# Kernel tuning notes

Hardware: AMD Instinct MI355X
Metric: run time of the kernel (lower is better)

## Reference

```python
import math
import jax, jax.numpy as jnp
import numpy as np

L, H, K, NH, V, DFF = 6, 512, 512, 8, 64, 1024
B, T, S = 8, 512, 512
PAD = 0


def _ln(x, g, b, eps=1e-5):
    m = jnp.mean(x, -1, keepdims=True)
    v = jnp.mean((x - m) ** 2, -1, keepdims=True)
    return (x - m) * jax.lax.rsqrt(v + eps) * g + b


def _mha(Q, Kin, Vin, mask, wq, bq, wk, bk, wv, bv, wo, bo, g, b):
    # weights stored [in, out]
    B_, Tq, Hd = Q.shape
    dk = wq.shape[1] // NH
    dv = wv.shape[1] // NH
    q = (Q @ wq + bq).reshape(B_, Tq, NH, dk).transpose(0, 2, 1, 3)
    k = (Kin @ wk + bk).reshape(B_, -1, NH, dk).transpose(0, 2, 1, 3)
    v = (Vin @ wv + bv).reshape(B_, -1, NH, dv).transpose(0, 2, 1, 3)
    scores = jnp.einsum('bhqd,bhkd->bhqk', q, k) / jnp.sqrt(jnp.float32(dk))
    scores = jnp.where(mask[:, None, :, :], jnp.float32(-1e9), scores)
    attn = jax.nn.softmax(scores, axis=-1)
    ctx = jnp.einsum('bhqk,bhkd->bhqd', attn, v).transpose(0, 2, 1, 3).reshape(B_, Tq, Hd)
    return _ln(ctx @ wo + bo + Q, g, b)


def _pe(t, d):
    pos = jnp.arange(t, dtype=jnp.float32)[:, None]
    div = jnp.exp(jnp.arange(0, d, 2, dtype=jnp.float32) * (-math.log(10000.0) / d))
    pe = jnp.zeros((t, d), jnp.float32)
    pe = pe.at[:, 0::2].set(jnp.sin(pos * div)).at[:, 1::2].set(jnp.cos(pos * div))
    return pe


def setup_inputs() -> dict:
    key = jax.random.key(0)
    ks = iter(jax.random.split(key, 40))
    nrm = lambda shape, s=0.02: jax.random.normal(next(ks), shape, jnp.float32) * s
    inp = {
        'smiles_index': jax.random.randint(next(ks), (B, T), 0, V, dtype=jnp.int32),
        'enc_outputs': jax.random.normal(next(ks), (B, S, H), jnp.float32),
        'enc_pad_mask': jnp.zeros((B, 1, S), bool),
        'tgt_len': T,
        'mol_emb': nrm((V, H), 1.0).at[PAD].set(0.0),  # padding_idx=0 row zeroed
        # self-attn stacks [L, ...]
        'sa_wq': nrm((L, H, K)), 'sa_bq': jnp.zeros((L, K)),
        'sa_wk': nrm((L, H, K)), 'sa_bk': jnp.zeros((L, K)),
        'sa_wv': nrm((L, H, H)), 'sa_bv': jnp.zeros((L, H)),
        'sa_wo': nrm((L, H, H)), 'sa_bo': jnp.zeros((L, H)),
        'ln1_g': jnp.ones((L, H)), 'ln1_b': jnp.zeros((L, H)),
        # cross-attn stacks
        'ea_wq': nrm((L, H, K)), 'ea_bq': jnp.zeros((L, K)),
        'ea_wk': nrm((L, H, K)), 'ea_bk': jnp.zeros((L, K)),
        'ea_wv': nrm((L, H, H)), 'ea_bv': jnp.zeros((L, H)),
        'ea_wo': nrm((L, H, H)), 'ea_bo': jnp.zeros((L, H)),
        'ln2_g': jnp.ones((L, H)), 'ln2_b': jnp.zeros((L, H)),
        # conv1x1 FFN == per-position linear
        'c1_w': nrm((L, H, DFF)), 'c1_b': jnp.zeros((L, DFF)),
        'c2_w': nrm((L, DFF, H)), 'c2_b': jnp.zeros((L, H)),
        'ln3_g': jnp.ones((L, H)), 'ln3_b': jnp.zeros((L, H)),
    }
    return inp


def reference(smiles_index, enc_outputs, enc_pad_mask, tgt_len, mol_emb,
              sa_wq, sa_bq, sa_wk, sa_bk, sa_wv, sa_bv, sa_wo, sa_bo, ln1_g, ln1_b,
              ea_wq, ea_bq, ea_wk, ea_bk, ea_wv, ea_bv, ea_wo, ea_bo, ln2_g, ln2_b,
              c1_w, c1_b, c2_w, c2_b, ln3_g, ln3_b):
    b, t = smiles_index.shape
    s = enc_outputs.shape[1]
    # embeddings + sinusoidal positional encoding (dropout is identity in eval)
    x = mol_emb[smiles_index] + _pe(t, mol_emb.shape[1])[None]
    # masks: pad (key == pad_id) OR causal upper-triangular
    pad = (smiles_index == PAD)[:, None, :]                 # [B,1,T] -> broadcast over queries
    causal = jnp.triu(jnp.ones((t, t), bool), 1)[None]      # [1,T,T]
    self_mask = pad | causal                                # [B,T,T]
    enc_mask = jnp.broadcast_to(enc_pad_mask, (b, t, s))    # [B,T,S]
    for l in range(L):
        x = _mha(x, x, x, self_mask,
                 sa_wq[l], sa_bq[l], sa_wk[l], sa_bk[l], sa_wv[l], sa_bv[l],
                 sa_wo[l], sa_bo[l], ln1_g[l], ln1_b[l])
        x = _mha(x, enc_outputs, enc_outputs, enc_mask,
                 ea_wq[l], ea_bq[l], ea_wk[l], ea_bk[l], ea_wv[l], ea_bv[l],
                 ea_wo[l], ea_bo[l], ln2_g[l], ln2_b[l])
        h = jax.nn.relu(x @ c1_w[l] + c1_b[l])
        y = h @ c2_w[l] + c2_b[l]
        x = _ln(y + x, ln3_g[l], ln3_b[l])
    return x
```

## Files before the change

### kernel.cpp

```cpp
#include <hip/hip_runtime.h>
#include <hip/hip_bf16.h>
#include <math.h>

#define NL   6
#define HD   512
#define NHD  8
#define DK   64
#define DFFN 1024
#define NB   8
#define TT   512
#define MROWS (NB*TT)

typedef __hip_bfloat16 bf16;
typedef __attribute__((ext_vector_type(8))) short short8v;
typedef __attribute__((ext_vector_type(4))) short short4v;
typedef __attribute__((ext_vector_type(4))) float f32x4;

__device__ __forceinline__ float wave_sum(float v) {
#pragma unroll
  for (int off = 32; off; off >>= 1) v += __shfl_xor(v, off);
  return v;
}
__device__ __forceinline__ unsigned short f2bf(float x) {
  __hip_bfloat16 h = __float2bfloat16(x);
  return *reinterpret_cast<unsigned short*>(&h);
}

__global__ __launch_bounds__(256)
void wprep_kernel(const float* __restrict__ W, bf16* __restrict__ Wt, int Kd, int Nd,
                  int dstRowOff, int dstSlabRows) {
  __shared__ float t[32][33];
  const size_t src = (size_t)blockIdx.z * Kd * Nd;
  const size_t dst = (size_t)blockIdx.z * dstSlabRows * Kd;
  const int n0 = blockIdx.x * 32, k0 = blockIdx.y * 32;
  const int tx = threadIdx.x & 31, ty = threadIdx.x >> 5;
#pragma unroll
  for (int j = 0; j < 4; ++j)
    t[ty + j * 8][tx] = W[src + (size_t)(k0 + ty + j * 8) * Nd + n0 + tx];
  __syncthreads();
#pragma unroll
  for (int j = 0; j < 4; ++j)
    Wt[dst + (size_t)(dstRowOff + n0 + ty + j * 8) * Kd + k0 + tx] =
        __float2bfloat16(t[tx][ty + j * 8]);
}

__global__ __launch_bounds__(256)
void bcat_kernel(const float* __restrict__ b0, const float* __restrict__ b1,
                 const float* __restrict__ b2, float* __restrict__ out, int nseg) {
  const int l = blockIdx.x;
  const int stride = 512 * nseg;
  for (int i = threadIdx.x; i < stride; i += 256) {
    const int seg = i >> 9, off = i & 511;
    const float* src = seg == 0 ? b0 : (seg == 1 ? b1 : b2);
    out[(size_t)l * stride + i] = src[(size_t)l * 512 + off];
  }
}

__global__ __launch_bounds__(256)
void cvtbf16_kernel(const float* __restrict__ in, unsigned short* __restrict__ out) {
  const int i = (blockIdx.x * 256 + threadIdx.x) * 4;
  float4 v = *(const float4*)(in + i);
  out[i + 0] = f2bf(v.x); out[i + 1] = f2bf(v.y);
  out[i + 2] = f2bf(v.z); out[i + 3] = f2bf(v.w);
}

__global__ __launch_bounds__(256)
void embed_pe_kernel(const int* __restrict__ idx, const float* __restrict__ emb,
                     float* __restrict__ x, unsigned short* __restrict__ xb) {
  const int row = blockIdx.x;
  const int t = row & (TT - 1);
  const int tok = idx[row];
  const float cdiv = -0.017988946009466842f;
#pragma unroll
  for (int e0 = 0; e0 < 2; ++e0) {
    const int e = threadIdx.x + e0 * 256;
    const float div = __expf((float)(e & ~1) * cdiv);
    const float ang = (float)t * div;
    const float pe = (e & 1) ? cosf(ang) : sinf(ang);
    const float v = emb[(size_t)tok * HD + e] + pe;
    x[(size_t)row * HD + e] = v;
    xb[(size_t)row * HD + e] = f2bf(v);
  }
}

__device__ __forceinline__ void gemm_compute(const char* As, const char* Bs,
                                             int wm, int wn, int lane,
                                             f32x4 (&acc)[2][2]) {
  const int rsw = (lane & 7) << 4;
  const int csel = (lane >> 4) * 16;
  short8v af[2][2], bfr[2][2];
#pragma unroll
  for (int m = 0; m < 2; ++m)
#pragma unroll
    for (int kk = 0; kk < 2; ++kk) {
      const int row = wm * 32 + m * 16 + (lane & 15);
      af[m][kk] = *(const short8v*)(As + row * 128 + ((kk * 64 + csel) ^ rsw));
    }
#pragma unroll
  for (int n = 0; n < 2; ++n)
#pragma unroll
    for (int kk = 0; kk < 2; ++kk) {
      const int row = wn * 32 + n * 16 + (lane & 15);
      bfr[n][kk] = *(const short8v*)(Bs + row * 128 + ((kk * 64 + csel) ^ rsw));
    }
#pragma unroll
  for (int m = 0; m < 2; ++m)
#pragma unroll
    for (int n = 0; n < 2; ++n) {
      acc[m][n] = __builtin_amdgcn_mfma_f32_16x16x32_bf16(af[m][0], bfr[n][0], acc[m][n], 0, 0, 0);
      acc[m][n] = __builtin_amdgcn_mfma_f32_16x16x32_bf16(af[m][1], bfr[n][1], acc[m][n], 0, 0, 0);
    }
}

template<int OUT_BF16, int RELU>
__global__ __launch_bounds__(256)
void mgemm_kernel(const bf16* __restrict__ A, const bf16* __restrict__ Bt,
                  const float* __restrict__ bias, float* __restrict__ Cf,
                  unsigned short* __restrict__ Cb, int M, int N, int K) {
  __shared__ __attribute__((aligned(16))) char As[64 * 128];
  __shared__ __attribute__((aligned(16))) char Bs[64 * 128];

  const int tid = threadIdx.x;
  const int w = tid >> 6, lane = tid & 63;
  const int wm = w >> 1, wn = w & 1;
  const int m0 = blockIdx.x * 64, n0 = blockIdx.y * 64;

  const int sr = w * 16 + (lane >> 3);
  const int scol = (lane & 7) * 16;
  const int swc = scol ^ ((sr & 7) << 4);
  const bf16* ga0 = A + (size_t)(m0 + sr) * K + (scol >> 1);
  const bf16* ga1 = A + (size_t)(m0 + sr + 8) * K + (scol >> 1);
  const bf16* gb0 = Bt + (size_t)(n0 + sr) * K + (scol >> 1);
  const bf16* gb1 = Bt + (size_t)(n0 + sr + 8) * K + (scol >> 1);
  char* la0 = As + sr * 128 + swc;
  char* la1 = As + (sr + 8) * 128 + swc;
  char* lb0 = Bs + sr * 128 + swc;
  char* lb1 = Bs + (sr + 8) * 128 + swc;

  f32x4 acc[2][2] = {};

  short8v ra0 = *(const short8v*)ga0, ra1 = *(const short8v*)ga1;
  short8v rb0 = *(const short8v*)gb0, rb1 = *(const short8v*)gb1;
  short8v sa0, sa1, sb0, sb1;

  for (int k0 = 0; k0 < K; k0 += 128) {
    __syncthreads();
    *(short8v*)la0 = ra0; *(short8v*)la1 = ra1;
    *(short8v*)lb0 = rb0; *(short8v*)lb1 = rb1;
    __syncthreads();
    sa0 = *(const short8v*)(ga0 + k0 + 64); sa1 = *(const short8v*)(ga1 + k0 + 64);
    sb0 = *(const short8v*)(gb0 + k0 + 64); sb1 = *(const short8v*)(gb1 + k0 + 64);
    gemm_compute(As, Bs, wm, wn, lane, acc);
    __syncthreads();
    *(short8v*)la0 = sa0; *(short8v*)la1 = sa1;
    *(short8v*)lb0 = sb0; *(short8v*)lb1 = sb1;
    __syncthreads();
    if (k0 + 128 < K) {
      ra0 = *(const short8v*)(ga0 + k0 + 128); ra1 = *(const short8v*)(ga1 + k0 + 128);
      rb0 = *(const short8v*)(gb0 + k0 + 128); rb1 = *(const short8v*)(gb1 + k0 + 128);
    }
    gemm_compute(As, Bs, wm, wn, lane, acc);
  }

  const int crow = (lane >> 4) * 4;
  const int ccol = lane & 15;
#pragma unroll
  for (int m = 0; m < 2; ++m)
#pragma unroll
    for (int n = 0; n < 2; ++n) {
      const int gr = m0 + wm * 32 + m * 16 + crow;
      const int gc = n0 + wn * 32 + n * 16 + ccol;
      const float bs = bias[gc];
#pragma unroll
      for (int r = 0; r < 4; ++r) {
        float v = acc[m][n][r] + bs;
        if (RELU) v = fmaxf(v, 0.f);
        if (OUT_BF16) Cb[(size_t)(gr + r) * N + gc] = f2bf(v);
        else          Cf[(size_t)(gr + r) * N + gc] = v;
      }
    }
}

template<int CAUSAL>
__global__ __launch_bounds__(512)
void mattn_kernel(const unsigned short* __restrict__ q, const unsigned short* __restrict__ kgl,
                  const unsigned short* __restrict__ vgl, unsigned short* __restrict__ ctx,
                  const int* __restrict__ idx, const unsigned char* __restrict__ emask,
                  int qstride, int kvstride) {
  __shared__ __attribute__((aligned(16))) unsigned short kt[64 * 64];
  __shared__ __attribute__((aligned(16))) unsigned short vt[64 * 64];
  __shared__ __attribute__((aligned(16))) unsigned short pl[8][16 * 64];
  __shared__ float km[64];

  const int bh = blockIdx.x;
  const int b = bh >> 3, h = bh & 7;
  const int qbase = blockIdx.y * 128;
  const int tid = threadIdx.x, w = tid >> 6, lane = tid & 63;
  const int l4 = lane & 15, g = lane >> 4;

  const unsigned short* qp = q + (size_t)(b * TT + qbase + w * 16 + l4) * qstride + h * DK + g * 8;
  short8v aq0 = *(const short8v*)qp;
  short8v aq1 = *(const short8v*)(qp + 32);

  float m_r[4], l_r[4];
  f32x4 acc_o[4];
#pragma unroll
  for (int r = 0; r < 4; ++r) { m_r[r] = -1e30f; l_r[r] = 0.f; }
#pragma unroll
  for (int f = 0; f < 4; ++f) acc_o[f] = (f32x4){0.f, 0.f, 0.f, 0.f};

  const int kvEnd = CAUSAL ? (qbase + 128) : TT;
  for (int kt0 = 0; kt0 < kvEnd; kt0 += 64) {
    __syncthreads();
    if (tid < 64) {
      const int kp = b * TT + kt0 + tid;
      const bool mk = CAUSAL ? (idx[kp] == 0) : (emask[kp] != 0);
      km[tid] = mk ? -1e9f : 0.f;
    }
    {
      const int r = tid >> 3, c8 = tid & 7;
      const unsigned short* kp = kgl + (size_t)(b * TT + kt0 + r) * kvstride + h * DK + c8 * 8;
      short8v kv = *(const short8v*)kp;
      *(short8v*)((char*)kt + r * 128 + ((c8 * 16) ^ ((r & 7) << 4))) = kv;
    }
    {
      const int k2 = (tid & 31) * 2;
      const int d4 = (tid >> 5) * 4;
      const unsigned short* vp0 = vgl + (size_t)(b * TT + kt0 + k2) * kvstride + h * DK + d4;
      const unsigned short* vp1 = vp0 + kvstride;
      short4v v0 = *(const short4v*)vp0;
      short4v v1 = *(const short4v*)vp1;
#pragma unroll
      for (int j = 0; j < 4; ++j) {
        const int d = d4 + j;
        const unsigned pk = ((unsigned)(unsigned short)v0[j]) | (((unsigned)(unsigned short)v1[j]) << 16);
        *(unsigned*)((char*)vt + d * 128 + ((k2 * 2) ^ ((d & 7) << 4))) = pk;
      }
    }
    __syncthreads();

    if (!(CAUSAL && kt0 > qbase + w * 16 + 15)) {
      const bool diag = CAUSAL && (kt0 + 64 > qbase + w * 16);

      f32x4 s4[4];
      __builtin_amdgcn_s_setprio(1);
#pragma unroll
      for (int f = 0; f < 4; ++f) {
        const int krow = f * 16 + l4;
        const int sw = (krow & 7) << 4;
        short8v bk0 = *(const short8v*)((const char*)kt + krow * 128 + ((g * 16) ^ sw));
        short8v bk1 = *(const short8v*)((const char*)kt + krow * 128 + ((64 + g * 16) ^ sw));
        f32x4 a = {};
        a = __builtin_amdgcn_mfma_f32_16x16x32_bf16(aq0, bk0, a, 0, 0, 0);
        a = __builtin_amdgcn_mfma_f32_16x16x32_bf16(aq1, bk1, a, 0, 0, 0);
        s4[f] = a;
      }
      __builtin_amdgcn_s_setprio(0);

      float kmb[4];
#pragma unroll
      for (int f = 0; f < 4; ++f) kmb[f] = km[f * 16 + l4];

      float sc_r[4];
#pragma unroll
      for (int r = 0; r < 4; ++r) {
        const int qpos = qbase + w * 16 + g * 4 + r;
        float sf[4];
#pragma unroll
        for (int f = 0; f < 4; ++f) sf[f] = fmaf(s4[f][r], 0.125f, kmb[f]);
        if (diag) {
#pragma unroll
          for (int f = 0; f < 4; ++f) {
            const int kpos = kt0 + f * 16 + l4;
            sf[f] = (kpos > qpos) ? -1e9f : sf[f];
          }
        }
        float mx = fmaxf(fmaxf(sf[0], sf[1]), fmaxf(sf[2], sf[3]));
#pragma unroll
        for (int off = 8; off; off >>= 1) mx = fmaxf(mx, __shfl_xor(mx, off));
        const float mn = fmaxf(m_r[r], mx);
        const float sc = __expf(m_r[r] - mn);
        m_r[r] = mn;
        sc_r[r] = sc;
        float ps = 0.f;
        const int prow = g * 4 + r;
        const int psw = (prow & 7) << 4;
#pragma unroll
        for (int f = 0; f < 4; ++f) {
          const float p = __expf(sf[f] - mn);
          ps += p;
          *(unsigned short*)((char*)pl[w] + prow * 128 + ((f * 32 + l4 * 2) ^ psw)) = f2bf(p);
        }
#pragma unroll
        for (int off = 8; off; off >>= 1) ps += __shfl_xor(ps, off);
        l_r[r] = l_r[r] * sc + ps;
      }

#pragma unroll
      for (int f = 0; f < 4; ++f)
#pragma unroll
        for (int r = 0; r < 4; ++r) acc_o[f][r] *= sc_r[r];

      const int asw = (l4 & 7) << 4;
      short8v pa0 = *(const short8v*)((const char*)pl[w] + l4 * 128 + ((g * 16) ^ asw));
      short8v pa1 = *(const short8v*)((const char*)pl[w] + l4 * 128 + ((g * 16 + 64) ^ asw));
      __builtin_amdgcn_s_setprio(1);
#pragma unroll
      for (int f = 0; f < 4; ++f) {
        const int drow = f * 16 + l4;
        const int sw = (drow & 7) << 4;
        short8v vb0 = *(const short8v*)((const char*)vt + drow * 128 + ((g * 16) ^ sw));
        short8v vb1 = *(const short8v*)((const char*)vt + drow * 128 + ((g * 16 + 64) ^ sw));
        acc_o[f] = __builtin_amdgcn_mfma_f32_16x16x32_bf16(pa0, vb0, acc_o[f], 0, 0, 0);
        acc_o[f] = __builtin_amdgcn_mfma_f32_16x16x32_bf16(pa1, vb1, acc_o[f], 0, 0, 0);
      }
      __builtin_amdgcn_s_setprio(0);
    }
  }

  float rl[4];
#pragma unroll
  for (int r = 0; r < 4; ++r) rl[r] = 1.f / l_r[r];
#pragma unroll
  for (int f = 0; f < 4; ++f)
#pragma unroll
    for (int r = 0; r < 4; ++r) {
      const int row = qbase + w * 16 + g * 4 + r;
      const int col = h * DK + f * 16 + l4;
      ctx[(size_t)(b * TT + row) * HD + col] = f2bf(acc_o[f][r] * rl[r]);
    }
}

__global__ __launch_bounds__(256)
void ln_kernel(const float* __restrict__ y, const float* __restrict__ res,
               float* __restrict__ out, unsigned short* __restrict__ outb,
               const float* __restrict__ g, const float* __restrict__ bta) {
  const int row = blockIdx.x;
  const int tid = threadIdx.x;
  const int w = tid >> 6, lane = tid & 63;
  const float* yr = y + (size_t)row * HD;
  const float* rr = res + (size_t)row * HD;

  float v0 = yr[tid] + rr[tid];
  float v1 = yr[tid + 256] + rr[tid + 256];

  __shared__ float red[4];
  float s = wave_sum(v0 + v1);
  if (lane == 0) red[w] = s;
  __syncthreads();
  const float mean = (red[0] + red[1] + red[2] + red[3]) * (1.f / HD);
  __syncthreads();

  const float d0 = v0 - mean, d1 = v1 - mean;
  float qv = wave_sum(d0 * d0 + d1 * d1);
  if (lane == 0) red[w] = qv;
  __syncthreads();
  const float var = (red[0] + red[1] + red[2] + red[3]) * (1.f / HD);
  const float rstd = rsqrtf(var + 1e-5f);

  const float o0 = d0 * rstd * g[tid] + bta[tid];
  const float o1 = d1 * rstd * g[tid + 256] + bta[tid + 256];
  out[(size_t)row * HD + tid] = o0;
  out[(size_t)row * HD + tid + 256] = o1;
  outb[(size_t)row * HD + tid] = f2bf(o0);
  outb[(size_t)row * HD + tid + 256] = f2bf(o1);
}

extern "C" void kernel_launch(void* const* d_in, const int* in_sizes, int n_in,
                              void* d_out, int out_size, void* d_ws, size_t ws_size,
                              hipStream_t stream) {
  const int* idx = (const int*)d_in[0];
  const float* enc = (const float*)d_in[1];
  const unsigned char* emask = (const unsigned char*)d_in[2];
  const float* emb = (const float*)d_in[4];
  const float* sa_wq = (const float*)d_in[5];
  const float* sa_bq = (const float*)d_in[6];
  const float* sa_wk = (const float*)d_in[7];
  const float* sa_bk = (const float*)d_in[8];
  const float* sa_wv = (const float*)d_in[9];
  const float* sa_bv = (const float*)d_in[10];
  const float* sa_wo = (const float*)d_in[11];
  const float* sa_bo = (const float*)d_in[12];
  const float* ln1g = (const float*)d_in[13];
  const float* ln1b = (const float*)d_in[14];
  const float* ea_wq = (const float*)d_in[15];
  const float* ea_bq = (const float*)d_in[16];
  const float* ea_wk = (const float*)d_in[17];
  const float* ea_bk = (const float*)d_in[18];
  const float* ea_wv = (const float*)d_in[19];
  const float* ea_bv = (const float*)d_in[20];
  const float* ea_wo = (const float*)d_in[21];
  const float* ea_bo = (const float*)d_in[22];
  const float* ln2g = (const float*)d_in[23];
  const float* ln2b = (const float*)d_in[24];
  const float* c1w = (const float*)d_in[25];
  const float* c1b = (const float*)d_in[26];
  const float* c2w = (const float*)d_in[27];
  const float* c2b = (const float*)d_in[28];
  const float* ln3g = (const float*)d_in[29];
  const float* ln3b = (const float*)d_in[30];

  const size_t MH = (size_t)MROWS * HD;
  const size_t SQ = (size_t)HD * HD;
  char* ws = (char*)d_ws;
  float*          x    = (float*)(ws + 0);
  unsigned short* xb   = (unsigned short*)(ws + (8u << 20));
  unsigned short* qkvb = (unsigned short*)(ws + (12u << 20));
  unsigned short* qcb  = (unsigned short*)(ws + (24u << 20));
  unsigned short* kvb  = (unsigned short*)(ws + (28u << 20));
  unsigned short* cxb  = (unsigned short*)(ws + (36u << 20));
  float*          yb   = (float*)(ws + (40u << 20));
  unsigned short* encb = (unsigned short*)(ws + (56u << 20));
  bf16*           wt   = (bf16*)(ws + (60u << 20));
  float*          bcS  = (float*)(ws + (98u << 20));
  float*          bcKV = (float*)(ws + (99u << 20));
  unsigned short* hb   = qkvb;

  bf16* t_saqkv = wt;
  bf16* t_sao   = wt + 18 * SQ;
  bf16* t_eaq   = wt + 24 * SQ;
  bf16* t_eakv  = wt + 30 * SQ;
  bf16* t_eao   = wt + 42 * SQ;
  bf16* t_c1    = wt + 48 * SQ;
  bf16* t_c2    = wt + 60 * SQ;

  const dim3 blk(256);
  const dim3 blk512(512);
  const dim3 gQKV(MROWS / 64, 1536 / 64);
  const dim3 g1024(MROWS / 64, 1024 / 64);
  const dim3 g512(MROWS / 64, 512 / 64);
  const dim3 attng(NB * NHD, TT / 128);

  wprep_kernel<<<dim3(16, 16, NL), blk, 0, stream>>>(sa_wq, t_saqkv, HD, HD, 0, 1536);
  wprep_kernel<<<dim3(16, 16, NL), blk, 0, stream>>>(sa_wk, t_saqkv, HD, HD, 512, 1536);
  wprep_kernel<<<dim3(16, 16, NL), blk, 0, stream>>>(sa_wv, t_saqkv, HD, HD, 1024, 1536);
  wprep_kernel<<<dim3(16, 16, NL), blk, 0, stream>>>(sa_wo, t_sao, HD, HD, 0, 512);
  wprep_kernel<<<dim3(16, 16, NL), blk, 0, stream>>>(ea_wq, t_eaq, HD, HD, 0, 512);
  wprep_kernel<<<dim3(16, 16, NL), blk, 0, stream>>>(ea_wk, t_eakv, HD, HD, 0, 1024);
  wprep_kernel<<<dim3(16, 16, NL), blk, 0, stream>>>(ea_wv, t_eakv, HD, HD, 512, 1024);
  wprep_kernel<<<dim3(16, 16, NL), blk, 0, stream>>>(ea_wo, t_eao, HD, HD, 0, 512);
  wprep_kernel<<<dim3(32, 16, NL), blk, 0, stream>>>(c1w, t_c1, HD, DFFN, 0, 1024);
  wprep_kernel<<<dim3(16, 32, NL), blk, 0, stream>>>(c2w, t_c2, DFFN, HD, 0, 512);
  bcat_kernel<<<NL, blk, 0, stream>>>(sa_bq, sa_bk, sa_bv, bcS, 3);
  bcat_kernel<<<NL, blk, 0, stream>>>(ea_bk, ea_bv, nullptr, bcKV, 2);
  cvtbf16_kernel<<<MH / 1024, blk, 0, stream>>>(enc, encb);

  embed_pe_kernel<<<MROWS, blk, 0, stream>>>(idx, emb, x, xb);

  for (int l = 0; l < NL; ++l) {
    const size_t b512 = (size_t)l * HD;
    const size_t bFF = (size_t)l * DFFN;

    mgemm_kernel<1, 0><<<gQKV, blk, 0, stream>>>(
        (const bf16*)xb, t_saqkv + (size_t)l * 3 * SQ, bcS + (size_t)l * 1536,
        nullptr, qkvb, MROWS, 1536, HD);
    mattn_kernel<1><<<attng, blk512, 0, stream>>>(qkvb, qkvb + 512, qkvb + 1024, cxb,
                                                  idx, emask, 1536, 1536);
    mgemm_kernel<0, 0><<<g512, blk, 0, stream>>>(
        (const bf16*)cxb, t_sao + (size_t)l * SQ, sa_bo + b512, yb, nullptr, MROWS, HD, HD);
    ln_kernel<<<MROWS, blk, 0, stream>>>(yb, x, x, xb, ln1g + b512, ln1b + b512);

    mgemm_kernel<1, 0><<<g512, blk, 0, stream>>>(
        (const bf16*)xb, t_eaq + (size_t)l * SQ, ea_bq + b512, nullptr, qcb, MROWS, HD, HD);
    mgemm_kernel<1, 0><<<g1024, blk, 0, stream>>>(
        (const bf16*)encb, t_eakv + (size_t)l * 2 * SQ, bcKV + (size_t)l * 1024,
        nullptr, kvb, MROWS, 1024, HD);
    mattn_kernel<0><<<attng, blk512, 0, stream>>>(qcb, kvb, kvb + 512, cxb,
                                                  idx, emask, 512, 1024);
    mgemm_kernel<0, 0><<<g512, blk, 0, stream>>>(
        (const bf16*)cxb, t_eao + (size_t)l * SQ, ea_bo + b512, yb, nullptr, MROWS, HD, HD);
    ln_kernel<<<MROWS, blk, 0, stream>>>(yb, x, x, xb, ln2g + b512, ln2b + b512);

    mgemm_kernel<1, 1><<<g1024, blk, 0, stream>>>(
        (const bf16*)xb, t_c1 + (size_t)l * 2 * SQ, c1b + bFF, nullptr, hb, MROWS, DFFN, HD);
    mgemm_kernel<0, 0><<<g512, blk, 0, stream>>>(
        (const bf16*)hb, t_c2 + (size_t)l * 2 * SQ, c2b + b512, yb, nullptr, MROWS, HD, DFFN);
    ln_kernel<<<MROWS, blk, 0, stream>>>(yb, x, x, xb, ln3g + b512, ln3b + b512);
  }

  hipMemcpyAsync(d_out, x, MH * sizeof(float), hipMemcpyDeviceToDevice, stream);
}
```

Baseline: 874.3 us.

## Fuse residual add into GEMM epilogue, prefetch attention K/V tiles, batch weight prep

The output-projection and FFN2 GEMMs now add the residual in their epilogue, so the layernorm kernel reads one input instead of two. The attention kernel loads the next K/V tile and mask into registers while the current tile is being computed, overlapping global loads with MFMA work. The eight square-weight transposes become one launch and the two bias concatenations become another, reducing launch count. Register pressure in the attention kernel rises from holding the prefetch registers.

```diff
diff --git a/kernel.cpp b/kernel.cpp
--- a/kernel.cpp
+++ b/kernel.cpp
@@ -10,6 +10,7 @@
 #define NB   8
 #define TT   512
 #define MROWS (NB*TT)
+#define SQC  262144
 
 typedef __hip_bfloat16 bf16;
 typedef __attribute__((ext_vector_type(8))) short short8v;
@@ -26,12 +27,34 @@
   return *reinterpret_cast<unsigned short*>(&h);
 }
 
-__global__ __launch_bounds__(256)
-void wprep_kernel(const float* __restrict__ W, bf16* __restrict__ Wt, int Kd, int Nd,
-                  int dstRowOff, int dstSlabRows) {
+struct Srcs8 { const float* s[8]; };
+__global__ __launch_bounds__(256)
+void wprep8_kernel(Srcs8 srcs, bf16* __restrict__ wt) {
+  const int z = blockIdx.z;
+  const int which = z & 7, l = z >> 3;
+  const long long baseT[8] = {0, 0, 0, 18LL*SQC, 24LL*SQC, 30LL*SQC, 30LL*SQC, 42LL*SQC};
+  const long long lstrT[8] = {3LL*SQC, 3LL*SQC, 3LL*SQC, SQC, SQC, 2LL*SQC, 2LL*SQC, SQC};
+  const int rowOffT[8] = {0, 512, 1024, 0, 0, 0, 512, 0};
+
+  __shared__ float t[32][33];
+  const float* W = srcs.s[which] + (size_t)l * SQC;
+  bf16* dst = wt + baseT[which] + (size_t)l * lstrT[which] + (size_t)rowOffT[which] * HD;
+  const int n0 = blockIdx.x * 32, k0 = blockIdx.y * 32;
+  const int tx = threadIdx.x & 31, ty = threadIdx.x >> 5;
+#pragma unroll
+  for (int j = 0; j < 4; ++j)
+    t[ty + j * 8][tx] = W[(size_t)(k0 + ty + j * 8) * HD + n0 + tx];
+  __syncthreads();
+#pragma unroll
+  for (int j = 0; j < 4; ++j)
+    dst[(size_t)(n0 + ty + j * 8) * HD + k0 + tx] = __float2bfloat16(t[tx][ty + j * 8]);
+}
+
+__global__ __launch_bounds__(256)
+void wprep_kernel(const float* __restrict__ W, bf16* __restrict__ Wt, int Kd, int Nd) {
   __shared__ float t[32][33];
   const size_t src = (size_t)blockIdx.z * Kd * Nd;
-  const size_t dst = (size_t)blockIdx.z * dstSlabRows * Kd;
+  const size_t dst = (size_t)blockIdx.z * Kd * Nd;
   const int n0 = blockIdx.x * 32, k0 = blockIdx.y * 32;
   const int tx = threadIdx.x & 31, ty = threadIdx.x >> 5;
 #pragma unroll
@@ -40,19 +63,26 @@
   __syncthreads();
 #pragma unroll
   for (int j = 0; j < 4; ++j)
-    Wt[dst + (size_t)(dstRowOff + n0 + ty + j * 8) * Kd + k0 + tx] =
-        __float2bfloat16(t[tx][ty + j * 8]);
-}
-
-__global__ __launch_bounds__(256)
-void bcat_kernel(const float* __restrict__ b0, const float* __restrict__ b1,
-                 const float* __restrict__ b2, float* __restrict__ out, int nseg) {
+    Wt[dst + (size_t)(n0 + ty + j * 8) * Kd + k0 + tx] = __float2bfloat16(t[tx][ty + j * 8]);
+}
+
+__global__ __launch_bounds__(256)
+void bcat2_kernel(const float* __restrict__ b0, const float* __restrict__ b1,
+                  const float* __restrict__ b2, const float* __restrict__ c0,
+                  const float* __restrict__ c1, float* __restrict__ outS,
+                  float* __restrict__ outKV) {
   const int l = blockIdx.x;
-  const int stride = 512 * nseg;
-  for (int i = threadIdx.x; i < stride; i += 256) {
-    const int seg = i >> 9, off = i & 511;
-    const float* src = seg == 0 ? b0 : (seg == 1 ? b1 : b2);
-    out[(size_t)l * stride + i] = src[(size_t)l * 512 + off];
+  if (blockIdx.y == 0) {
+    for (int i = threadIdx.x; i < 1536; i += 256) {
+      const int seg = i >> 9, off = i & 511;
+      const float* src = seg == 0 ? b0 : (seg == 1 ? b1 : b2);
+      outS[(size_t)l * 1536 + i] = src[(size_t)l * 512 + off];
+    }
+  } else {
+    for (int i = threadIdx.x; i < 1024; i += 256) {
+      const float* src = (i >> 9) == 0 ? c0 : c1;
+      outKV[(size_t)l * 1024 + i] = src[(size_t)l * 512 + (i & 511)];
+    }
   }
 }
 
@@ -112,11 +142,12 @@
     }
 }
 
-template<int OUT_BF16, int RELU>
+template<int OUT_BF16, int RELU, int ADDRES>
 __global__ __launch_bounds__(256)
 void mgemm_kernel(const bf16* __restrict__ A, const bf16* __restrict__ Bt,
-                  const float* __restrict__ bias, float* __restrict__ Cf,
-                  unsigned short* __restrict__ Cb, int M, int N, int K) {
+                  const float* __restrict__ bias, const float* __restrict__ res,
+                  float* __restrict__ Cf, unsigned short* __restrict__ Cb,
+                  int M, int N, int K) {
   __shared__ __attribute__((aligned(16))) char As[64 * 128];
   __shared__ __attribute__((aligned(16))) char Bs[64 * 128];
 
@@ -175,6 +206,7 @@
       for (int r = 0; r < 4; ++r) {
         float v = acc[m][n][r] + bs;
         if (RELU) v = fmaxf(v, 0.f);
+        if (ADDRES) v += res[(size_t)(gr + r) * N + gc];
         if (OUT_BF16) Cb[(size_t)(gr + r) * N + gc] = f2bf(v);
         else          Cf[(size_t)(gr + r) * N + gc] = v;
       }
@@ -202,6 +234,21 @@
   short8v aq0 = *(const short8v*)qp;
   short8v aq1 = *(const short8v*)(qp + 32);
 
+  const int sr_k = tid >> 3, sc8 = tid & 7;
+  const unsigned short* kbp = kgl + (size_t)(b * TT + sr_k) * kvstride + h * DK + sc8 * 8;
+  const int k2 = (tid & 31) * 2, d4 = (tid >> 5) * 4;
+  const unsigned short* vbp0 = vgl + (size_t)(b * TT + k2) * kvstride + h * DK + d4;
+  const unsigned short* vbp1 = vbp0 + kvstride;
+
+  short8v rk = *(const short8v*)kbp;
+  short4v rv0 = *(const short4v*)vbp0;
+  short4v rv1 = *(const short4v*)vbp1;
+  float mreg = 0.f;
+  if (tid < 64) {
+    const int kp = b * TT + tid;
+    mreg = (CAUSAL ? (idx[kp] == 0) : (emask[kp] != 0)) ? -1e9f : 0.f;
+  }
+
   float m_r[4], l_r[4];
   f32x4 acc_o[4];
 #pragma unroll
@@ -212,32 +259,26 @@
   const int kvEnd = CAUSAL ? (qbase + 128) : TT;
   for (int kt0 = 0; kt0 < kvEnd; kt0 += 64) {
     __syncthreads();
-    if (tid < 64) {
-      const int kp = b * TT + kt0 + tid;
-      const bool mk = CAUSAL ? (idx[kp] == 0) : (emask[kp] != 0);
-      km[tid] = mk ? -1e9f : 0.f;
-    }
-    {
-      const int r = tid >> 3, c8 = tid & 7;
-      const unsigned short* kp = kgl + (size_t)(b * TT + kt0 + r) * kvstride + h * DK + c8 * 8;
-      short8v kv = *(const short8v*)kp;
-      *(short8v*)((char*)kt + r * 128 + ((c8 * 16) ^ ((r & 7) << 4))) = kv;
-    }
-    {
-      const int k2 = (tid & 31) * 2;
-      const int d4 = (tid >> 5) * 4;
-      const unsigned short* vp0 = vgl + (size_t)(b * TT + kt0 + k2) * kvstride + h * DK + d4;
-      const unsigned short* vp1 = vp0 + kvstride;
-      short4v v0 = *(const short4v*)vp0;
-      short4v v1 = *(const short4v*)vp1;
-#pragma unroll
-      for (int j = 0; j < 4; ++j) {
-        const int d = d4 + j;
-        const unsigned pk = ((unsigned)(unsigned short)v0[j]) | (((unsigned)(unsigned short)v1[j]) << 16);
-        *(unsigned*)((char*)vt + d * 128 + ((k2 * 2) ^ ((d & 7) << 4))) = pk;
+    if (tid < 64) km[tid] = mreg;
+    *(short8v*)((char*)kt + sr_k * 128 + ((sc8 * 16) ^ ((sr_k & 7) << 4))) = rk;
+#pragma unroll
+    for (int j = 0; j < 4; ++j) {
+      const int d = d4 + j;
+      const unsigned pk = ((unsigned)(unsigned short)rv0[j]) | (((unsigned)(unsigned short)rv1[j]) << 16);
+      *(unsigned*)((char*)vt + d * 128 + ((k2 * 2) ^ ((d & 7) << 4))) = pk;
+    }
+    __syncthreads();
+
+    if (kt0 + 64 < kvEnd) {
+      const size_t off = (size_t)(kt0 + 64) * kvstride;
+      rk = *(const short8v*)(kbp + off);
+      rv0 = *(const short4v*)(vbp0 + off);
+      rv1 = *(const short4v*)(vbp1 + off);
+      if (tid < 64) {
+        const int kp = b * TT + kt0 + 64 + tid;
+        mreg = (CAUSAL ? (idx[kp] == 0) : (emask[kp] != 0)) ? -1e9f : 0.f;
       }
     }
-    __syncthreads();
 
     if (!(CAUSAL && kt0 > qbase + w * 16 + 15)) {
       const bool diag = CAUSAL && (kt0 + 64 > qbase + w * 16);
@@ -332,17 +373,16 @@
 }
 
 __global__ __launch_bounds__(256)
-void ln_kernel(const float* __restrict__ y, const float* __restrict__ res,
-               float* __restrict__ out, unsigned short* __restrict__ outb,
-               const float* __restrict__ g, const float* __restrict__ bta) {
+void ln2_kernel(const float* __restrict__ v, float* __restrict__ out,
+                unsigned short* __restrict__ outb,
+                const float* __restrict__ g, const float* __restrict__ bta) {
   const int row = blockIdx.x;
   const int tid = threadIdx.x;
   const int w = tid >> 6, lane = tid & 63;
-  const float* yr = y + (size_t)row * HD;
-  const float* rr = res + (size_t)row * HD;
-
-  float v0 = yr[tid] + rr[tid];
-  float v1 = yr[tid + 256] + rr[tid + 256];
+  const size_t ro = (size_t)row * HD;
+
+  float v0 = v[ro + tid];
+  float v1 = v[ro + tid + 256];
 
   __shared__ float red[4];
   float s = wave_sum(v0 + v1);
@@ -360,10 +400,10 @@
 
   const float o0 = d0 * rstd * g[tid] + bta[tid];
   const float o1 = d1 * rstd * g[tid + 256] + bta[tid + 256];
-  out[(size_t)row * HD + tid] = o0;
-  out[(size_t)row * HD + tid + 256] = o1;
-  outb[(size_t)row * HD + tid] = f2bf(o0);
-  outb[(size_t)row * HD + tid + 256] = f2bf(o1);
+  out[ro + tid] = o0;
+  out[ro + tid + 256] = o1;
+  outb[ro + tid] = f2bf(o0);
+  outb[ro + tid + 256] = f2bf(o1);
 }
 
 extern "C" void kernel_launch(void* const* d_in, const int* in_sizes, int n_in,
@@ -401,7 +441,7 @@
   const float* ln3b = (const float*)d_in[30];
 
   const size_t MH = (size_t)MROWS * HD;
-  const size_t SQ = (size_t)HD * HD;
+  const size_t SQ = (size_t)SQC;
   char* ws = (char*)d_ws;
   float*          x    = (float*)(ws + 0);
   unsigned short* xb   = (unsigned short*)(ws + (8u << 20));
@@ -431,18 +471,13 @@
   const dim3 g512(MROWS / 64, 512 / 64);
   const dim3 attng(NB * NHD, TT / 128);
 
-  wprep_kernel<<<dim3(16, 16, NL), blk, 0, stream>>>(sa_wq, t_saqkv, HD, HD, 0, 1536);
-  wprep_kernel<<<dim3(16, 16, NL), blk, 0, stream>>>(sa_wk, t_saqkv, HD, HD, 512, 1536);
-  wprep_kernel<<<dim3(16, 16, NL), blk, 0, stream>>>(sa_wv, t_saqkv, HD, HD, 1024, 1536);
-  wprep_kernel<<<dim3(16, 16, NL), blk, 0, stream>>>(sa_wo, t_sao, HD, HD, 0, 512);
-  wprep_kernel<<<dim3(16, 16, NL), blk, 0, stream>>>(ea_wq, t_eaq, HD, HD, 0, 512);
-  wprep_kernel<<<dim3(16, 16, NL), blk, 0, stream>>>(ea_wk, t_eakv, HD, HD, 0, 1024);
-  wprep_kernel<<<dim3(16, 16, NL), blk, 0, stream>>>(ea_wv, t_eakv, HD, HD, 512, 1024);
-  wprep_kernel<<<dim3(16, 16, NL), blk, 0, stream>>>(ea_wo, t_eao, HD, HD, 0, 512);
-  wprep_kernel<<<dim3(32, 16, NL), blk, 0, stream>>>(c1w, t_c1, HD, DFFN, 0, 1024);
-  wprep_kernel<<<dim3(16, 32, NL), blk, 0, stream>>>(c2w, t_c2, DFFN, HD, 0, 512);
-  bcat_kernel<<<NL, blk, 0, stream>>>(sa_bq, sa_bk, sa_bv, bcS, 3);
-  bcat_kernel<<<NL, blk, 0, stream>>>(ea_bk, ea_bv, nullptr, bcKV, 2);
+  Srcs8 s8;
+  s8.s[0] = sa_wq; s8.s[1] = sa_wk; s8.s[2] = sa_wv; s8.s[3] = sa_wo;
+  s8.s[4] = ea_wq; s8.s[5] = ea_wk; s8.s[6] = ea_wv; s8.s[7] = ea_wo;
+  wprep8_kernel<<<dim3(16, 16, 48), blk, 0, stream>>>(s8, wt);
+  wprep_kernel<<<dim3(32, 16, NL), blk, 0, stream>>>(c1w, t_c1, HD, DFFN);
+  wprep_kernel<<<dim3(16, 32, NL), blk, 0, stream>>>(c2w, t_c2, DFFN, HD);
+  bcat2_kernel<<<dim3(NL, 2), blk, 0, stream>>>(sa_bq, sa_bk, sa_bv, ea_bk, ea_bv, bcS, bcKV);
   cvtbf16_kernel<<<MH / 1024, blk, 0, stream>>>(enc, encb);
 
   embed_pe_kernel<<<MROWS, blk, 0, stream>>>(idx, emb, x, xb);
@@ -451,31 +486,31 @@
     const size_t b512 = (size_t)l * HD;
     const size_t bFF = (size_t)l * DFFN;
 
-    mgemm_kernel<1, 0><<<gQKV, blk, 0, stream>>>(
+    mgemm_kernel<1, 0, 0><<<gQKV, blk, 0, stream>>>(
         (const bf16*)xb, t_saqkv + (size_t)l * 3 * SQ, bcS + (size_t)l * 1536,
-        nullptr, qkvb, MROWS, 1536, HD);
+        nullptr, nullptr, qkvb, MROWS, 1536, HD);
     mattn_kernel<1><<<attng, blk512, 0, stream>>>(qkvb, qkvb + 512, qkvb + 1024, cxb,
                                                   idx, emask, 1536, 1536);
-    mgemm_kernel<0, 0><<<g512, blk, 0, stream>>>(
-        (const bf16*)cxb, t_sao + (size_t)l * SQ, sa_bo + b512, yb, nullptr, MROWS, HD, HD);
-    ln_kernel<<<MROWS, blk, 0, stream>>>(yb, x, x, xb, ln1g + b512, ln1b + b512);
-
-    mgemm_kernel<1, 0><<<g512, blk, 0, stream>>>(
-        (const bf16*)xb, t_eaq + (size_t)l * SQ, ea_bq + b512, nullptr, qcb, MROWS, HD, HD);
-    mgemm_kernel<1, 0><<<g1024, blk, 0, stream>>>(
+    mgemm_kernel<0, 0, 1><<<g512, blk, 0, stream>>>(
+        (const bf16*)cxb, t_sao + (size_t)l * SQ, sa_bo + b512, x, yb, nullptr, MROWS, HD, HD);
+    ln2_kernel<<<MROWS, blk, 0, stream>>>(yb, x, xb, ln1g + b512, ln1b + b512);
+
+    mgemm_kernel<1, 0, 0><<<g512, blk, 0, stream>>>(
+        (const bf16*)xb, t_eaq + (size_t)l * SQ, ea_bq + b512, nullptr, nullptr, qcb, MROWS, HD, HD);
+    mgemm_kernel<1, 0, 0><<<g1024, blk, 0, stream>>>(
         (const bf16*)encb, t_eakv + (size_t)l * 2 * SQ, bcKV + (size_t)l * 1024,
-        nullptr, kvb, MROWS, 1024, HD);
+        nullptr, nullptr, kvb, MROWS, 1024, HD);
     mattn_kernel<0><<<attng, blk512, 0, stream>>>(qcb, kvb, kvb + 512, cxb,
                                                   idx, emask, 512, 1024);
-    mgemm_kernel<0, 0><<<g512, blk, 0, stream>>>(
-        (const bf16*)cxb, t_eao + (size_t)l * SQ, ea_bo + b512, yb, nullptr, MROWS, HD, HD);
-    ln_kernel<<<MROWS, blk, 0, stream>>>(yb, x, x, xb, ln2g + b512, ln2b + b512);
-
-    mgemm_kernel<1, 1><<<g1024, blk, 0, stream>>>(
-        (const bf16*)xb, t_c1 + (size_t)l * 2 * SQ, c1b + bFF, nullptr, hb, MROWS, DFFN, HD);
-    mgemm_kernel<0, 0><<<g512, blk, 0, stream>>>(
-        (const bf16*)hb, t_c2 + (size_t)l * 2 * SQ, c2b + b512, yb, nullptr, MROWS, HD, DFFN);
-    ln_kernel<<<MROWS, blk, 0, stream>>>(yb, x, x, xb, ln3g + b512, ln3b + b512);
+    mgemm_kernel<0, 0, 1><<<g512, blk, 0, stream>>>(
+        (const bf16*)cxb, t_eao + (size_t)l * SQ, ea_bo + b512, x, yb, nullptr, MROWS, HD, HD);
+    ln2_kernel<<<MROWS, blk, 0, stream>>>(yb, x, xb, ln2g + b512, ln2b + b512);
+
+    mgemm_kernel<1, 1, 0><<<g1024, blk, 0, stream>>>(
+        (const bf16*)xb, t_c1 + (size_t)l * 2 * SQ, c1b + bFF, nullptr, nullptr, hb, MROWS, DFFN, HD);
+    mgemm_kernel<0, 0, 1><<<g512, blk, 0, stream>>>(
+        (const bf16*)hb, t_c2 + (size_t)l * 2 * SQ, c2b + b512, x, yb, nullptr, MROWS, HD, DFFN);
+    ln2_kernel<<<MROWS, blk, 0, stream>>>(yb, x, xb, ln3g + b512, ln3b + b512);
   }
 
   hipMemcpyAsync(d_out, x, MH * sizeof(float), hipMemcpyDeviceToDevice, stream);
```

New measurement: 868.3 us. About the same (-0.7%).
